# Kernel tuning notes

Hardware: AMD Instinct MI355X
Metric: run time of the kernel (lower is better)

## Reference

```python
import jax, jax.numpy as jnp
import numpy as np

B, P, PLOIDY = 8, 5000, 2
NALLELES, NPOS, D = 16, 20000, 64


def setup_inputs() -> dict:
    key = jax.random.key(0)
    k1, k2, k3, k4, k5 = jax.random.split(key, 5)
    alleles = jax.random.randint(k1, (B, P, PLOIDY), 0, NALLELES, dtype=jnp.int32)
    positions = jax.random.randint(k2, (B, P), 0, NPOS, dtype=jnp.int32)
    allele_table = jax.random.normal(k3, (NALLELES, D), dtype=jnp.float32)
    kernel_table = jax.random.normal(k4, (NPOS, D * D), dtype=jnp.float32)
    bias_table = jax.random.normal(k5, (NPOS, D), dtype=jnp.float32)
    return {"alleles": alleles, "positions": positions,
            "allele_table": allele_table, "kernel_table": kernel_table,
            "bias_table": bias_table}


def reference(alleles, positions, allele_table, kernel_table, bias_table):
    # gather allele embeddings and sum over ploidy: [B,P,ploidy,D] -> [B,P,D]
    a = allele_table[alleles].sum(axis=-2)
    # per-position weight matrix: [B,P,D,D]
    kernel = kernel_table[positions].reshape(positions.shape[0], positions.shape[1], D, D)
    bias = bias_table[positions]                       # [B,P,D]
    # batched 1xD @ DxD matmul, fused with bias add
    out = jnp.einsum('bpd,bpde->bpe', a, kernel) + bias
    return out  # activation is None (linear)
```

## Files before the change

kernel.cpp:

```cpp
#include <hip/hip_runtime.h>

#define BB 8
#define PP 5000
#define DD 64
#define NBP (BB * PP)
#define NPOSC 20000
#define GRID_POS (NPOSC / 4)
#define CHUNK 80

static __device__ __forceinline__ float4 f4add(float4 a, float4 b) {
    return make_float4(a.x + b.x, a.y + b.y, a.z + b.z, a.w + b.w);
}

__global__ __launch_bounds__(256) void hist_kernel(
    const int* __restrict__ positions, int* __restrict__ hist)
{
    const int tid = blockIdx.x * 256 + threadIdx.x;
    if (tid < NBP) atomicAdd(&hist[positions[tid]], 1);
}

__global__ __launch_bounds__(256) void scan_kernel(
    const int* __restrict__ hist, int* __restrict__ offs,
    int* __restrict__ cursor)
{
    __shared__ int lsum[256];
    const int t = threadIdx.x;
    const int base = t * CHUNK;
    int run = 0;
    for (int j = 0; j < CHUNK; ++j) {
        const int idx = base + j;
        if (idx < NPOSC) run += hist[idx];
    }
    lsum[t] = run;
    __syncthreads();
    if (t == 0) {
        int acc = 0;
        for (int i = 0; i < 256; ++i) { const int x = lsum[i]; lsum[i] = acc; acc += x; }
    }
    __syncthreads();
    int acc = lsum[t];
    for (int j = 0; j < CHUNK; ++j) {
        const int idx = base + j;
        if (idx < NPOSC) {
            offs[idx]   = acc;
            cursor[idx] = acc;
            acc += hist[idx];
        }
    }
    if (t == 255) offs[NPOSC] = acc;
}

__global__ __launch_bounds__(256) void scatter_kernel(
    const int* __restrict__ positions, int* __restrict__ cursor,
    int* __restrict__ order)
{
    const int tid = blockIdx.x * 256 + threadIdx.x;
    if (tid < NBP) {
        const int idx = atomicAdd(&cursor[positions[tid]], 1);
        order[idx] = tid;
    }
}

__global__ __launch_bounds__(256) void allele_embed_kernel(
    const int* __restrict__ alleles,
    const float* __restrict__ allele_table,
    const float4* __restrict__ ktab4,
    const float4* __restrict__ btab4,
    const int* __restrict__ offs,
    const int* __restrict__ order,
    float4* __restrict__ out4)
{
    const int wave = threadIdx.x >> 6;
    const int lane = threadIdx.x & 63;
    const int work = (blockIdx.x & 7) * (GRID_POS / 8) + (blockIdx.x >> 3);
    const int pos  = work * 4 + wave;

    const int start = offs[pos];
    const int end   = offs[pos + 1];
    if (start == end) return;

    const float4* __restrict__ krow = ktab4 + (size_t)pos * (DD * DD / 4);
    const int dg = lane >> 4;
    const float4 bv = btab4[(size_t)pos * (DD / 4) + (lane & 15)];

    for (int c = start; c < end; c += 4) {
        const int m = end - c;
        const int bp0 = order[c];
        const int bp1 = (m > 1) ? order[c + 1] : bp0;
        const int bp2 = (m > 2) ? order[c + 2] : bp0;
        const int bp3 = (m > 3) ? order[c + 3] : bp0;

        const float a0 = allele_table[alleles[bp0 * 2] * DD + lane]
                       + allele_table[alleles[bp0 * 2 + 1] * DD + lane];
        const float a1 = allele_table[alleles[bp1 * 2] * DD + lane]
                       + allele_table[alleles[bp1 * 2 + 1] * DD + lane];
        const float a2 = allele_table[alleles[bp2 * 2] * DD + lane]
                       + allele_table[alleles[bp2 * 2 + 1] * DD + lane];
        const float a3 = allele_table[alleles[bp3 * 2] * DD + lane]
                       + allele_table[alleles[bp3 * 2 + 1] * DD + lane];

        float4 acc0 = make_float4(0.f, 0.f, 0.f, 0.f);
        float4 acc1 = acc0, acc2 = acc0, acc3 = acc0;
#pragma unroll
        for (int i = 0; i < 16; ++i) {
            const int d = i * 4 + dg;
            const float4 kv = krow[i * 64 + lane];
            const float d0 = __shfl(a0, d, 64);
            const float d1 = __shfl(a1, d, 64);
            const float d2 = __shfl(a2, d, 64);
            const float d3 = __shfl(a3, d, 64);
            acc0.x += d0 * kv.x; acc0.y += d0 * kv.y; acc0.z += d0 * kv.z; acc0.w += d0 * kv.w;
            acc1.x += d1 * kv.x; acc1.y += d1 * kv.y; acc1.z += d1 * kv.z; acc1.w += d1 * kv.w;
            acc2.x += d2 * kv.x; acc2.y += d2 * kv.y; acc2.z += d2 * kv.z; acc2.w += d2 * kv.w;
            acc3.x += d3 * kv.x; acc3.y += d3 * kv.y; acc3.z += d3 * kv.z; acc3.w += d3 * kv.w;
        }

#pragma unroll
        for (int off = 16; off <= 32; off <<= 1) {
            acc0.x += __shfl_xor(acc0.x, off, 64); acc0.y += __shfl_xor(acc0.y, off, 64);
            acc0.z += __shfl_xor(acc0.z, off, 64); acc0.w += __shfl_xor(acc0.w, off, 64);
            acc1.x += __shfl_xor(acc1.x, off, 64); acc1.y += __shfl_xor(acc1.y, off, 64);
            acc1.z += __shfl_xor(acc1.z, off, 64); acc1.w += __shfl_xor(acc1.w, off, 64);
            acc2.x += __shfl_xor(acc2.x, off, 64); acc2.y += __shfl_xor(acc2.y, off, 64);
            acc2.z += __shfl_xor(acc2.z, off, 64); acc2.w += __shfl_xor(acc2.w, off, 64);
            acc3.x += __shfl_xor(acc3.x, off, 64); acc3.y += __shfl_xor(acc3.y, off, 64);
            acc3.z += __shfl_xor(acc3.z, off, 64); acc3.w += __shfl_xor(acc3.w, off, 64);
        }

        if (lane < 16) {
            out4[(size_t)bp0 * (DD / 4) + lane] = f4add(acc0, bv);
            if (m > 1) out4[(size_t)bp1 * (DD / 4) + lane] = f4add(acc1, bv);
            if (m > 2) out4[(size_t)bp2 * (DD / 4) + lane] = f4add(acc2, bv);
            if (m > 3) out4[(size_t)bp3 * (DD / 4) + lane] = f4add(acc3, bv);
        }
    }
}

extern "C" void kernel_launch(void* const* d_in, const int* in_sizes, int n_in,
                              void* d_out, int out_size, void* d_ws, size_t ws_size,
                              hipStream_t stream) {
    const int*   alleles      = (const int*)d_in[0];
    const int*   positions    = (const int*)d_in[1];
    const float* allele_table = (const float*)d_in[2];
    const float4* ktab4       = (const float4*)d_in[3];
    const float4* btab4       = (const float4*)d_in[4];
    float4* out4              = (float4*)d_out;

    int* hist   = (int*)d_ws;
    int* offs   = hist + NPOSC;
    int* cursor = offs + (NPOSC + 1);
    int* order  = cursor + NPOSC;

    hipMemsetAsync(hist, 0, NPOSC * sizeof(int), stream);

    const int gprep = (NBP + 255) / 256;
    hist_kernel<<<gprep, 256, 0, stream>>>(positions, hist);
    scan_kernel<<<1, 256, 0, stream>>>(hist, offs, cursor);
    scatter_kernel<<<gprep, 256, 0, stream>>>(positions, cursor, order);

    allele_embed_kernel<<<GRID_POS, 256, 0, stream>>>(
        alleles, allele_table, ktab4, btab4, offs, order, out4);
}
```

Baseline: 499.2 us.

## Replace histogram-scan-scatter bucketing with fixed-slot claim plus overflow tail kernel

Drops the separate histogram and single-block scan kernels. One atomic claim pass writes each batch-position index into a fixed 16-slot bucket per table position, and entries past 16 go to an overflow list handled by a new tail kernel. It also adds a single-row fast path for positions used once. This removes two launches and the serial scan, in exchange for a third kernel launch and extra workspace.

```diff
diff --git a/kernel.cpp b/kernel.cpp
--- a/kernel.cpp
+++ b/kernel.cpp
@@ -5,59 +5,26 @@
 #define DD 64
 #define NBP (BB * PP)
 #define NPOSC 20000
+#define SLOTS 16
 #define GRID_POS (NPOSC / 4)
-#define CHUNK 80
 
 static __device__ __forceinline__ float4 f4add(float4 a, float4 b) {
     return make_float4(a.x + b.x, a.y + b.y, a.z + b.z, a.w + b.w);
 }
 
-__global__ __launch_bounds__(256) void hist_kernel(
-    const int* __restrict__ positions, int* __restrict__ hist)
-{
-    const int tid = blockIdx.x * 256 + threadIdx.x;
-    if (tid < NBP) atomicAdd(&hist[positions[tid]], 1);
-}
-
-__global__ __launch_bounds__(256) void scan_kernel(
-    const int* __restrict__ hist, int* __restrict__ offs,
-    int* __restrict__ cursor)
-{
-    __shared__ int lsum[256];
-    const int t = threadIdx.x;
-    const int base = t * CHUNK;
-    int run = 0;
-    for (int j = 0; j < CHUNK; ++j) {
-        const int idx = base + j;
-        if (idx < NPOSC) run += hist[idx];
-    }
-    lsum[t] = run;
-    __syncthreads();
-    if (t == 0) {
-        int acc = 0;
-        for (int i = 0; i < 256; ++i) { const int x = lsum[i]; lsum[i] = acc; acc += x; }
-    }
-    __syncthreads();
-    int acc = lsum[t];
-    for (int j = 0; j < CHUNK; ++j) {
-        const int idx = base + j;
-        if (idx < NPOSC) {
-            offs[idx]   = acc;
-            cursor[idx] = acc;
-            acc += hist[idx];
-        }
-    }
-    if (t == 255) offs[NPOSC] = acc;
-}
-
-__global__ __launch_bounds__(256) void scatter_kernel(
-    const int* __restrict__ positions, int* __restrict__ cursor,
-    int* __restrict__ order)
+__global__ __launch_bounds__(256) void claim_kernel(
+    const int* __restrict__ positions,
+    int* __restrict__ cnt,
+    int* __restrict__ ovf_cnt,
+    int* __restrict__ order2,
+    int* __restrict__ ovf)
 {
     const int tid = blockIdx.x * 256 + threadIdx.x;
     if (tid < NBP) {
-        const int idx = atomicAdd(&cursor[positions[tid]], 1);
-        order[idx] = tid;
+        const int p = positions[tid];
+        const int k = atomicAdd(&cnt[p], 1);
+        if (k < SLOTS) order2[p * SLOTS + k] = tid;
+        else           ovf[atomicAdd(ovf_cnt, 1)] = tid;
     }
 }
 
@@ -66,8 +33,8 @@
     const float* __restrict__ allele_table,
     const float4* __restrict__ ktab4,
     const float4* __restrict__ btab4,
-    const int* __restrict__ offs,
-    const int* __restrict__ order,
+    const int* __restrict__ cnt,
+    const int* __restrict__ order2,
     float4* __restrict__ out4)
 {
     const int wave = threadIdx.x >> 6;
@@ -75,20 +42,42 @@
     const int work = (blockIdx.x & 7) * (GRID_POS / 8) + (blockIdx.x >> 3);
     const int pos  = work * 4 + wave;
 
-    const int start = offs[pos];
-    const int end   = offs[pos + 1];
-    if (start == end) return;
+    int n = cnt[pos];
+    if (n == 0) return;
+    if (n > SLOTS) n = SLOTS;
 
     const float4* __restrict__ krow = ktab4 + (size_t)pos * (DD * DD / 4);
+    const int* __restrict__ slot = order2 + pos * SLOTS;
     const int dg = lane >> 4;
     const float4 bv = btab4[(size_t)pos * (DD / 4) + (lane & 15)];
 
-    for (int c = start; c < end; c += 4) {
-        const int m = end - c;
-        const int bp0 = order[c];
-        const int bp1 = (m > 1) ? order[c + 1] : bp0;
-        const int bp2 = (m > 2) ? order[c + 2] : bp0;
-        const int bp3 = (m > 3) ? order[c + 3] : bp0;
+    if (n == 1) {
+        const int bp = slot[0];
+        const float a = allele_table[alleles[bp * 2] * DD + lane]
+                      + allele_table[alleles[bp * 2 + 1] * DD + lane];
+        float4 acc = make_float4(0.f, 0.f, 0.f, 0.f);
+#pragma unroll
+        for (int i = 0; i < 16; ++i) {
+            const float ad = __shfl(a, i * 4 + dg, 64);
+            const float4 kv = krow[i * 64 + lane];
+            acc.x += ad * kv.x; acc.y += ad * kv.y;
+            acc.z += ad * kv.z; acc.w += ad * kv.w;
+        }
+#pragma unroll
+        for (int off = 16; off <= 32; off <<= 1) {
+            acc.x += __shfl_xor(acc.x, off, 64); acc.y += __shfl_xor(acc.y, off, 64);
+            acc.z += __shfl_xor(acc.z, off, 64); acc.w += __shfl_xor(acc.w, off, 64);
+        }
+        if (lane < 16) out4[(size_t)bp * (DD / 4) + lane] = f4add(acc, bv);
+        return;
+    }
+
+    for (int c = 0; c < n; c += 4) {
+        const int m = n - c;
+        const int bp0 = slot[c];
+        const int bp1 = (m > 1) ? slot[c + 1] : bp0;
+        const int bp2 = (m > 2) ? slot[c + 2] : bp0;
+        const int bp3 = (m > 3) ? slot[c + 3] : bp0;
 
         const float a0 = allele_table[alleles[bp0 * 2] * DD + lane]
                        + allele_table[alleles[bp0 * 2 + 1] * DD + lane];
@@ -114,7 +103,6 @@
             acc2.x += d2 * kv.x; acc2.y += d2 * kv.y; acc2.z += d2 * kv.z; acc2.w += d2 * kv.w;
             acc3.x += d3 * kv.x; acc3.y += d3 * kv.y; acc3.z += d3 * kv.z; acc3.w += d3 * kv.w;
         }
-
 #pragma unroll
         for (int off = 16; off <= 32; off <<= 1) {
             acc0.x += __shfl_xor(acc0.x, off, 64); acc0.y += __shfl_xor(acc0.y, off, 64);
@@ -126,12 +114,51 @@
             acc3.x += __shfl_xor(acc3.x, off, 64); acc3.y += __shfl_xor(acc3.y, off, 64);
             acc3.z += __shfl_xor(acc3.z, off, 64); acc3.w += __shfl_xor(acc3.w, off, 64);
         }
-
         if (lane < 16) {
             out4[(size_t)bp0 * (DD / 4) + lane] = f4add(acc0, bv);
             if (m > 1) out4[(size_t)bp1 * (DD / 4) + lane] = f4add(acc1, bv);
             if (m > 2) out4[(size_t)bp2 * (DD / 4) + lane] = f4add(acc2, bv);
             if (m > 3) out4[(size_t)bp3 * (DD / 4) + lane] = f4add(acc3, bv);
+        }
+    }
+}
+
+__global__ __launch_bounds__(256) void tail_kernel(
+    const int* __restrict__ alleles,
+    const int* __restrict__ positions,
+    const float* __restrict__ allele_table,
+    const float4* __restrict__ ktab4,
+    const float4* __restrict__ btab4,
+    const int* __restrict__ ovf_cnt,
+    const int* __restrict__ ovf,
+    float4* __restrict__ out4)
+{
+    const int nov  = *ovf_cnt;
+    const int lane = threadIdx.x & 63;
+    const int wid  = blockIdx.x * 4 + (threadIdx.x >> 6);
+    const int dg   = lane >> 4;
+    for (int i = wid; i < nov; i += 256) {
+        const int bp  = ovf[i];
+        const int pos = positions[bp];
+        const float a = allele_table[alleles[bp * 2] * DD + lane]
+                      + allele_table[alleles[bp * 2 + 1] * DD + lane];
+        const float4* krow = ktab4 + (size_t)pos * (DD * DD / 4);
+        float4 acc = make_float4(0.f, 0.f, 0.f, 0.f);
+#pragma unroll
+        for (int k = 0; k < 16; ++k) {
+            const float ad = __shfl(a, k * 4 + dg, 64);
+            const float4 kv = krow[k * 64 + lane];
+            acc.x += ad * kv.x; acc.y += ad * kv.y;
+            acc.z += ad * kv.z; acc.w += ad * kv.w;
+        }
+#pragma unroll
+        for (int off = 16; off <= 32; off <<= 1) {
+            acc.x += __shfl_xor(acc.x, off, 64); acc.y += __shfl_xor(acc.y, off, 64);
+            acc.z += __shfl_xor(acc.z, off, 64); acc.w += __shfl_xor(acc.w, off, 64);
+        }
+        if (lane < 16) {
+            const float4 bv = btab4[(size_t)pos * (DD / 4) + lane];
+            out4[(size_t)bp * (DD / 4) + lane] = f4add(acc, bv);
         }
     }
 }
@@ -146,18 +173,19 @@
     const float4* btab4       = (const float4*)d_in[4];
     float4* out4              = (float4*)d_out;
 
-    int* hist   = (int*)d_ws;
-    int* offs   = hist + NPOSC;
-    int* cursor = offs + (NPOSC + 1);
-    int* order  = cursor + NPOSC;
+    int* cnt     = (int*)d_ws;
+    int* ovf_cnt = cnt + NPOSC;
+    int* order2  = cnt + NPOSC + 32;
+    int* ovf     = order2 + NPOSC * SLOTS;
 
-    hipMemsetAsync(hist, 0, NPOSC * sizeof(int), stream);
+    hipMemsetAsync(cnt, 0, (NPOSC + 32) * sizeof(int), stream);
 
     const int gprep = (NBP + 255) / 256;
-    hist_kernel<<<gprep, 256, 0, stream>>>(positions, hist);
-    scan_kernel<<<1, 256, 0, stream>>>(hist, offs, cursor);
-    scatter_kernel<<<gprep, 256, 0, stream>>>(positions, cursor, order);
+    claim_kernel<<<gprep, 256, 0, stream>>>(positions, cnt, ovf_cnt, order2, ovf);
 
     allele_embed_kernel<<<GRID_POS, 256, 0, stream>>>(
-        alleles, allele_table, ktab4, btab4, offs, order, out4);
+        alleles, allele_table, ktab4, btab4, cnt, order2, out4);
+
+    tail_kernel<<<64, 256, 0, stream>>>(
+        alleles, positions, allele_table, ktab4, btab4, ovf_cnt, ovf, out4);
 }
```

Result: faster. 442.6 us (-11.3%).
